# Kernel optimization log

Hardware: AMD Instinct MI355X
Metric: run time of the kernel (lower is better)

The kernel has to match this reference:

```python
import jax, jax.numpy as jnp
import numpy as np

N = 50000        # nodes
E = 800000       # edges (avg degree 16)
IN_DIM = 64
OUT_DIM = 64
SLOPE = 0.01     # torch F.leaky_relu default negative_slope


def setup_inputs() -> dict:
    key = jax.random.key(0)
    ks = jax.random.split(key, 11)
    v = jax.random.normal(ks[0], (N, IN_DIM), dtype=jnp.float32)
    pre_w = jax.random.uniform(ks[1], (E, 1), dtype=jnp.float32)
    src = jax.random.randint(ks[2], (E,), 0, N)
    dst = jax.random.randint(ks[3], (E,), 0, N)
    # learned params (Linear weights, stored [out_features, in_features] like torch)
    si = 1.0 / np.sqrt(IN_DIM)
    so = 1.0 / np.sqrt(OUT_DIM)
    Wa  = jax.random.normal(ks[4], (OUT_DIM, IN_DIM), dtype=jnp.float32) * si
    a_l = jax.random.normal(ks[5], (1, OUT_DIM), dtype=jnp.float32) * so
    a_r = jax.random.normal(ks[6], (1, OUT_DIM), dtype=jnp.float32) * so
    Wg  = jax.random.normal(ks[7], (OUT_DIM, IN_DIM), dtype=jnp.float32) * si
    gl  = jax.random.normal(ks[8], (1, IN_DIM), dtype=jnp.float32) * si
    gm  = jax.random.normal(ks[9], (1, OUT_DIM), dtype=jnp.float32) * so
    gr  = jax.random.normal(ks[10], (1, IN_DIM), dtype=jnp.float32) * si
    return {"v": v, "pre_w": pre_w, "src": src, "dst": dst,
            "Wa": Wa, "a_l": a_l, "a_r": a_r, "Wg": Wg,
            "gl": gl, "gm": gm, "gr": gr}


def reference(v, pre_w, src, dst, Wa, a_l, a_r, Wg, gl, gm, gr):
    # node projection: z = Wa(v)
    z = v @ Wa.T                                            # [N, OUT]
    # edge attention: e = leaky_relu(a_l(pre_w * z_src) + a_r(z_dst))
    s_r = z @ a_r.T                                         # [N, 1] (node-level right score)
    z_src = z[src]                                          # [E, OUT]
    e = jax.nn.leaky_relu(((pre_w * z_src) @ a_l.T + s_r[dst])[:, 0], SLOPE)  # [E]
    # segment softmax over in-edges of each dst node
    seg_max = jax.ops.segment_max(e, dst, num_segments=N)
    seg_max = jnp.where(jnp.isneginf(seg_max), 0.0, seg_max)
    ex = jnp.exp(e - seg_max[dst])                          # [E]
    denom = jax.ops.segment_sum(ex, dst, num_segments=N)    # [N]
    alpha = ex / jnp.maximum(denom[dst], 1e-16)             # [E]
    # attention-weighted aggregation of projected src features
    h = jax.ops.segment_sum(alpha[:, None] * z_src, dst, num_segments=N)  # [N, OUT]
    # gate path: pwFeat = pre_w * v_src, max over Wg(pwFeat), mean over pwFeat
    pwFeat = pre_w * v[src]                                 # [E, IN]
    gateProj = pwFeat @ Wg.T                                # [E, OUT]
    maxFeat = jax.ops.segment_max(gateProj, dst, num_segments=N)
    maxFeat = jnp.where(jnp.isneginf(maxFeat), 0.0, maxFeat)  # [N, OUT]
    cnt = jax.ops.segment_sum(jnp.ones((E,), jnp.float32), dst, num_segments=N)
    meanFeat = jax.ops.segment_sum(pwFeat, dst, num_segments=N) / jnp.maximum(cnt, 1.0)[:, None]
    gate = jax.nn.sigmoid(v @ gl.T + maxFeat @ gm.T + meanFeat @ gr.T)  # [N, 1]
    h = gate * h
    return h.reshape(1, N, OUT_DIM)  # batch_size = 1
```

## Files before the change

kernel.cpp:

```cpp
#include <hip/hip_runtime.h>
#include <hip/hip_fp16.h>

#define DIM 64
#define SLOPE 0.01f
#define P1_CHUNK 4096
#define CAP 8192
#define LDH 72

typedef _Float16 half8 __attribute__((ext_vector_type(8)));
typedef float float4v __attribute__((ext_vector_type(4)));

__global__ __launch_bounds__(256) void node_proj(
    const float* __restrict__ v, const float* __restrict__ Wa,
    const float* __restrict__ Wg, const float* __restrict__ a_l,
    const float* __restrict__ a_r, const float* __restrict__ gl,
    const float* __restrict__ gr,
    __half2* __restrict__ zu,
    float* __restrict__ s_l, float* __restrict__ s_r,
    float* __restrict__ t_gr, float* __restrict__ g0, int N)
{
    __shared__ _Float16 vt[64 * LDH];
    __shared__ _Float16 wah[64 * LDH];
    __shared__ _Float16 wgh[64 * LDH];
    __shared__ _Float16 bx[16 * LDH];
    int tid = threadIdx.x;
    int base = blockIdx.x * 64;

    {
        int r = tid >> 2, i0 = (tid & 3) * 16;
        int n = base + r;
        _Float16* dv = &vt[r * LDH + i0];
        if (n < N) {
            const float4* sv = (const float4*)(v + (size_t)n * DIM + i0);
#pragma unroll
            for (int c = 0; c < 4; c++) {
                float4 q = sv[c];
                dv[4*c+0] = (_Float16)q.x; dv[4*c+1] = (_Float16)q.y;
                dv[4*c+2] = (_Float16)q.z; dv[4*c+3] = (_Float16)q.w;
            }
        } else {
#pragma unroll
            for (int c = 0; c < 16; c++) dv[c] = (_Float16)0.f;
        }
        const float4* sa = (const float4*)(Wa + (size_t)r * DIM + i0);
        const float4* sg = (const float4*)(Wg + (size_t)r * DIM + i0);
        _Float16* da = &wah[r * LDH + i0];
        _Float16* dg = &wgh[r * LDH + i0];
#pragma unroll
        for (int c = 0; c < 4; c++) {
            float4 qa = sa[c], qg = sg[c];
            da[4*c+0] = (_Float16)qa.x; da[4*c+1] = (_Float16)qa.y;
            da[4*c+2] = (_Float16)qa.z; da[4*c+3] = (_Float16)qa.w;
            dg[4*c+0] = (_Float16)qg.x; dg[4*c+1] = (_Float16)qg.y;
            dg[4*c+2] = (_Float16)qg.z; dg[4*c+3] = (_Float16)qg.w;
        }
        if (tid < 64)       bx[0 * LDH + tid] = (_Float16)gl[tid];
        else if (tid < 128) bx[1 * LDH + (tid - 64)] = (_Float16)gr[tid - 64];
        for (int x = tid; x < 12 * 64; x += 256)
            bx[(4 + (x >> 6)) * LDH + (x & 63)] = (_Float16)0.f;
    }
    __syncthreads();
    if (tid < 64) {
        int i = tid;
        float acc = 0.f;
        for (int k = 0; k < 64; k++) acc = fmaf(a_l[k], (float)wah[k * LDH + i], acc);
        bx[2 * LDH + i] = (_Float16)acc;
    } else if (tid < 128) {
        int i = tid - 64;
        float acc = 0.f;
        for (int k = 0; k < 64; k++) acc = fmaf(a_r[k], (float)wah[k * LDH + i], acc);
        bx[3 * LDH + i] = (_Float16)acc;
    }
    __syncthreads();

    int lane = tid & 63;
    int m0 = (tid >> 6) * 16;
    int rb = lane & 15;
    int q  = lane >> 4;

    half8 a_lo = *(const half8*)&vt[(m0 + rb) * LDH + q * 8];
    half8 a_hi = *(const half8*)&vt[(m0 + rb) * LDH + 32 + q * 8];

    float4v zacc[4], uacc[4], sacc;
#pragma unroll
    for (int tc = 0; tc < 4; tc++) { zacc[tc] = (float4v)0.f; uacc[tc] = (float4v)0.f; }
    sacc = (float4v)0.f;

#pragma unroll
    for (int tc = 0; tc < 4; tc++) {
        int c0 = tc * 16;
        half8 blo = *(const half8*)&wah[(c0 + rb) * LDH + q * 8];
        half8 bhi = *(const half8*)&wah[(c0 + rb) * LDH + 32 + q * 8];
        zacc[tc] = __builtin_amdgcn_mfma_f32_16x16x32_f16(a_lo, blo, zacc[tc], 0, 0, 0);
        zacc[tc] = __builtin_amdgcn_mfma_f32_16x16x32_f16(a_hi, bhi, zacc[tc], 0, 0, 0);
        half8 glo = *(const half8*)&wgh[(c0 + rb) * LDH + q * 8];
        half8 ghi = *(const half8*)&wgh[(c0 + rb) * LDH + 32 + q * 8];
        uacc[tc] = __builtin_amdgcn_mfma_f32_16x16x32_f16(a_lo, glo, uacc[tc], 0, 0, 0);
        uacc[tc] = __builtin_amdgcn_mfma_f32_16x16x32_f16(a_hi, ghi, uacc[tc], 0, 0, 0);
    }
    {
        half8 blo = *(const half8*)&bx[rb * LDH + q * 8];
        half8 bhi = *(const half8*)&bx[rb * LDH + 32 + q * 8];
        sacc = __builtin_amdgcn_mfma_f32_16x16x32_f16(a_lo, blo, sacc, 0, 0, 0);
        sacc = __builtin_amdgcn_mfma_f32_16x16x32_f16(a_hi, bhi, sacc, 0, 0, 0);
    }

#pragma unroll
    for (int r = 0; r < 4; r++) {
        int n = base + m0 + q * 4 + r;
        if (n < N) {
#pragma unroll
            for (int tc = 0; tc < 4; tc++)
                zu[(size_t)n * DIM + tc * 16 + rb] = __floats2half2_rn(zacc[tc][r], uacc[tc][r]);
        }
    }
    if (rb < 4) {
        float* arr = (rb == 0) ? g0 : (rb == 1) ? t_gr : (rb == 2) ? s_l : s_r;
#pragma unroll
        for (int r = 0; r < 4; r++) {
            int n = base + m0 + q * 4 + r;
            if (n < N) arr[n] = sacc[r];
        }
    }
}

__global__ __launch_bounds__(256) void bucket_scatter(
    const int* __restrict__ src, const int* __restrict__ dst,
    const float* __restrict__ pre_w,
    int* __restrict__ bcur0, uint2* __restrict__ tmp, int E)
{
    __shared__ int h[256], lcur[256], wbase[256];
    int t = threadIdx.x;
    h[t] = 0; lcur[t] = 0;
    __syncthreads();
    int e0 = blockIdx.x * P1_CHUNK;
    int e1 = e0 + P1_CHUNK; if (e1 > E) e1 = E;
    for (int e = e0 + t; e < e1; e += 256)
        atomicAdd(&h[dst[e] >> 8], 1);
    __syncthreads();
    int hv = h[t];
    wbase[t] = hv ? atomicAdd(&bcur0[t], hv) : 0;
    __syncthreads();
    for (int e = e0 + t; e < e1; e += 256) {
        int d = dst[e];
        int b = d >> 8;
        int pos = wbase[b] + atomicAdd(&lcur[b], 1);
        if (pos < CAP) {
            unsigned lo = ((unsigned)src[e] << 16) |
                          __half_as_ushort(__float2half_rn(pre_w[e]));
            uint2 r; r.x = lo; r.y = (unsigned)d;
            tmp[(size_t)b * CAP + pos] = r;
        }
    }
}

__global__ __launch_bounds__(256) void bucket_to_csr(
    const uint2* __restrict__ tmp, const int* __restrict__ bcur0,
    int* __restrict__ offs, int* __restrict__ deg,
    unsigned int* __restrict__ sp_s, int N)
{
    __shared__ int h[256], excl[256], cur[256], sc[256];
    int b = blockIdx.x;
    int t = threadIdx.x;
    int c = bcur0[t]; if (c > CAP) c = CAP;
    sc[t] = c;
    __syncthreads();
    for (int off = 1; off < 256; off <<= 1) {
        int y = (t >= off) ? sc[t - off] : 0;
        __syncthreads();
        sc[t] += y;
        __syncthreads();
    }
    int start = (b == 0) ? 0 : sc[b - 1];
    int bcnt = sc[b] - start;
    const uint2* reg = tmp + (size_t)b * CAP;
    h[t] = 0; cur[t] = 0;
    __syncthreads();
    for (int i = t; i < bcnt; i += 256)
        atomicAdd(&h[reg[i].y & 255], 1);
    __syncthreads();
    int x = h[t];
    excl[t] = x;
    __syncthreads();
    for (int off = 1; off < 256; off <<= 1) {
        int y = (t >= off) ? excl[t - off] : 0;
        __syncthreads();
        excl[t] += y;
        __syncthreads();
    }
    int ex = excl[t] - x;
    int n = (b << 8) + t;
    if (n < N) { offs[n] = start + ex; deg[n] = x; }
    __syncthreads();
    excl[t] = ex;
    __syncthreads();
    for (int i = t; i < bcnt; i += 256) {
        uint2 r = reg[i];
        int d8 = r.y & 255;
        int pos = start + excl[d8] + atomicAdd(&cur[d8], 1);
        sp_s[pos] = r.x;
    }
}

__global__ __launch_bounds__(256) void aggregate(
    const int* __restrict__ offs, const int* __restrict__ deg_a,
    const unsigned int* __restrict__ sp_s,
    const __half2* __restrict__ zu,
    const float* __restrict__ s_l, const float* __restrict__ s_r,
    const float* __restrict__ t_gr, const float* __restrict__ g0,
    const float* __restrict__ gm,
    float* __restrict__ out, int N)
{
    int n = __builtin_amdgcn_readfirstlane((blockIdx.x * 256 + threadIdx.x) >> 6);
    int k = threadIdx.x & 63;
    if (n >= N) return;
    int deg = deg_a[n];
    size_t outIdx = (size_t)n * DIM + k;
    if (deg == 0) { out[outIdx] = 0.f; return; }
    int start = offs[n];
    float srn = s_r[n];

    float m = -INFINITY, denom = 0.f, hk = 0.f, mfk = -INFINITY, msum = 0.f;
    for (int c0 = 0; c0 < deg; c0 += 64) {
        int cn = deg - c0; if (cn > 64) cn = 64;
        unsigned rec = 0;
        float ea = -INFINITY;
        if (k < cn) {
            rec = sp_s[start + c0 + k];
            float pw = __half2float(__ushort_as_half((unsigned short)(rec & 0xffffu)));
            ea = fmaf(pw, s_l[rec >> 16], srn);
            ea = ea > 0.f ? ea : SLOPE * ea;
            msum = fmaf(pw, t_gr[rec >> 16], msum);
        }
        float mc = ea;
#pragma unroll
        for (int off = 32; off; off >>= 1) mc = fmaxf(mc, __shfl_xor(mc, off, 64));
        float mnew = fmaxf(m, mc);
        float scale = __expf(m - mnew);
        float w = __expf(ea - mnew);
        float sw = w;
#pragma unroll
        for (int off = 32; off; off >>= 1) sw += __shfl_xor(sw, off, 64);
        denom = denom * scale + sw;
        hk *= scale;
        m = mnew;
        int j = 0;
        for (; j + 8 <= cn; j += 8) {
            unsigned r8[8]; float w8[8]; __half2 q8[8];
#pragma unroll
            for (int i = 0; i < 8; i++) {
                r8[i] = __shfl(rec, j + i, 64);
                w8[i] = __shfl(w, j + i, 64);
            }
#pragma unroll
            for (int i = 0; i < 8; i++) q8[i] = zu[(size_t)(r8[i] >> 16) * DIM + k];
#pragma unroll
            for (int i = 0; i < 8; i++) {
                float2 f = __half22float2(q8[i]);
                float pwj = __half2float(__ushort_as_half((unsigned short)(r8[i] & 0xffffu)));
                hk = fmaf(w8[i], f.x, hk);
                mfk = fmaxf(mfk, pwj * f.y);
            }
        }
        for (; j < cn; j++) {
            unsigned rj = __shfl(rec, j, 64);
            float wj = __shfl(w, j, 64);
            __half2 q = zu[(size_t)(rj >> 16) * DIM + k];
            float2 f = __half22float2(q);
            float pwj = __half2float(__ushort_as_half((unsigned short)(rj & 0xffffu)));
            hk = fmaf(wj, f.x, hk);
            mfk = fmaxf(mfk, pwj * f.y);
        }
    }
#pragma unroll
    for (int off = 32; off; off >>= 1) msum += __shfl_xor(msum, off, 64);
    float r = gm[k] * mfk;
#pragma unroll
    for (int off = 32; off; off >>= 1) r += __shfl_down(r, off, 64);
    r = __shfl(r, 0, 64);
    float meanDot = msum / (float)deg;
    float xg = g0[n] + r + meanDot;
    float gate = 1.f / (1.f + __expf(-xg));
    out[outIdx] = gate * hk / fmaxf(denom, 1e-16f);
}

extern "C" void kernel_launch(void* const* d_in, const int* in_sizes, int n_in,
                              void* d_out, int out_size, void* d_ws, size_t ws_size,
                              hipStream_t stream)
{
    const float* v     = (const float*)d_in[0];
    const float* pre_w = (const float*)d_in[1];
    const int*   src   = (const int*)d_in[2];
    const int*   dst   = (const int*)d_in[3];
    const float* Wa    = (const float*)d_in[4];
    const float* a_l   = (const float*)d_in[5];
    const float* a_r   = (const float*)d_in[6];
    const float* Wg    = (const float*)d_in[7];
    const float* gl    = (const float*)d_in[8];
    const float* gm    = (const float*)d_in[9];
    const float* gr    = (const float*)d_in[10];
    int N = in_sizes[0] / DIM;
    int E = in_sizes[2];
    int nbuck = (N + 255) >> 8;

    char* ws    = (char*)d_ws;
    __half2* zu = (__half2*)ws;
    float* s_l  = (float*)(ws + (size_t)N * DIM * 4);
    float* s_r  = s_l + N;
    float* t_gr = s_r + N;
    float* g0   = t_gr + N;
    int* offs   = (int*)(g0 + N);
    int* deg    = offs + N;
    int* bcur0  = deg + N;
    uint2* tmp  = (uint2*)(bcur0 + 256);
    unsigned int* sp_s = (unsigned int*)(tmp + (size_t)nbuck * CAP);

    hipMemsetAsync(bcur0, 0, 256 * sizeof(int), stream);

    node_proj<<<(N + 63) / 64, 256, 0, stream>>>(
        v, Wa, Wg, a_l, a_r, gl, gr, zu, s_l, s_r, t_gr, g0, N);

    bucket_scatter<<<(E + P1_CHUNK - 1) / P1_CHUNK, 256, 0, stream>>>(
        src, dst, pre_w, bcur0, tmp, E);

    bucket_to_csr<<<nbuck, 256, 0, stream>>>(
        tmp, bcur0, offs, deg, sp_s, N);

    aggregate<<<(N + 3) / 4, 256, 0, stream>>>(
        offs, deg, sp_s, zu, s_l, s_r, t_gr, g0, gm, (float*)d_out, N);
}
```

Baseline: 168.1 us.

## Merge node projection and bucket scatter into one launch; interleave s_l and t_gr

```diff
diff --git a/kernel.cpp b/kernel.cpp
--- a/kernel.cpp
+++ b/kernel.cpp
@@ -10,21 +10,54 @@
 typedef _Float16 half8 __attribute__((ext_vector_type(8)));
 typedef float float4v __attribute__((ext_vector_type(4)));
 
-__global__ __launch_bounds__(256) void node_proj(
+__global__ __launch_bounds__(256) void proj_scatter(
     const float* __restrict__ v, const float* __restrict__ Wa,
     const float* __restrict__ Wg, const float* __restrict__ a_l,
     const float* __restrict__ a_r, const float* __restrict__ gl,
     const float* __restrict__ gr,
-    __half2* __restrict__ zu,
-    float* __restrict__ s_l, float* __restrict__ s_r,
-    float* __restrict__ t_gr, float* __restrict__ g0, int N)
+    __half2* __restrict__ zu, float2* __restrict__ st,
+    float* __restrict__ s_r, float* __restrict__ g0,
+    const int* __restrict__ src, const int* __restrict__ dst,
+    const float* __restrict__ pre_w,
+    int* __restrict__ bcur0, uint2* __restrict__ tmp,
+    int N, int E, int scBlocks)
 {
-    __shared__ _Float16 vt[64 * LDH];
-    __shared__ _Float16 wah[64 * LDH];
-    __shared__ _Float16 wgh[64 * LDH];
-    __shared__ _Float16 bx[16 * LDH];
+    __shared__ char smem[(64 * 3 + 16) * LDH * 2];
     int tid = threadIdx.x;
-    int base = blockIdx.x * 64;
+
+    if (blockIdx.x < scBlocks) {
+        int* h    = (int*)smem;
+        int* lcur = h + 256;
+        int* wbase = lcur + 256;
+        h[tid] = 0; lcur[tid] = 0;
+        __syncthreads();
+        int e0 = blockIdx.x * P1_CHUNK;
+        int e1 = e0 + P1_CHUNK; if (e1 > E) e1 = E;
+        for (int e = e0 + tid; e < e1; e += 256)
+            atomicAdd(&h[dst[e] >> 8], 1);
+        __syncthreads();
+        int hv = h[tid];
+        wbase[tid] = hv ? atomicAdd(&bcur0[tid], hv) : 0;
+        __syncthreads();
+        for (int e = e0 + tid; e < e1; e += 256) {
+            int d = dst[e];
+            int b = d >> 8;
+            int pos = wbase[b] + atomicAdd(&lcur[b], 1);
+            if (pos < CAP) {
+                unsigned lo = ((unsigned)src[e] << 16) |
+                              __half_as_ushort(__float2half_rn(pre_w[e]));
+                uint2 r; r.x = lo; r.y = (unsigned)d;
+                tmp[(size_t)b * CAP + pos] = r;
+            }
+        }
+        return;
+    }
+
+    _Float16* vt  = (_Float16*)smem;
+    _Float16* wah = vt + 64 * LDH;
+    _Float16* wgh = wah + 64 * LDH;
+    _Float16* bx  = wgh + 64 * LDH;
+    int base = (blockIdx.x - scBlocks) * 64;
 
     {
         int r = tid >> 2, i0 = (tid & 3) * 16;
@@ -115,41 +148,16 @@
         }
     }
     if (rb < 4) {
-        float* arr = (rb == 0) ? g0 : (rb == 1) ? t_gr : (rb == 2) ? s_l : s_r;
 #pragma unroll
         for (int r = 0; r < 4; r++) {
             int n = base + m0 + q * 4 + r;
-            if (n < N) arr[n] = sacc[r];
-        }
-    }
-}
-
-__global__ __launch_bounds__(256) void bucket_scatter(
-    const int* __restrict__ src, const int* __restrict__ dst,
-    const float* __restrict__ pre_w,
-    int* __restrict__ bcur0, uint2* __restrict__ tmp, int E)
-{
-    __shared__ int h[256], lcur[256], wbase[256];
-    int t = threadIdx.x;
-    h[t] = 0; lcur[t] = 0;
-    __syncthreads();
-    int e0 = blockIdx.x * P1_CHUNK;
-    int e1 = e0 + P1_CHUNK; if (e1 > E) e1 = E;
-    for (int e = e0 + t; e < e1; e += 256)
-        atomicAdd(&h[dst[e] >> 8], 1);
-    __syncthreads();
-    int hv = h[t];
-    wbase[t] = hv ? atomicAdd(&bcur0[t], hv) : 0;
-    __syncthreads();
-    for (int e = e0 + t; e < e1; e += 256) {
-        int d = dst[e];
-        int b = d >> 8;
-        int pos = wbase[b] + atomicAdd(&lcur[b], 1);
-        if (pos < CAP) {
-            unsigned lo = ((unsigned)src[e] << 16) |
-                          __half_as_ushort(__float2half_rn(pre_w[e]));
-            uint2 r; r.x = lo; r.y = (unsigned)d;
-            tmp[(size_t)b * CAP + pos] = r;
+            if (n < N) {
+                float val = sacc[r];
+                if (rb == 0) g0[n] = val;
+                else if (rb == 1) st[n].y = val;
+                else if (rb == 2) st[n].x = val;
+                else s_r[n] = val;
+            }
         }
     }
 }
@@ -206,9 +214,8 @@
     const int* __restrict__ offs, const int* __restrict__ deg_a,
     const unsigned int* __restrict__ sp_s,
     const __half2* __restrict__ zu,
-    const float* __restrict__ s_l, const float* __restrict__ s_r,
-    const float* __restrict__ t_gr, const float* __restrict__ g0,
-    const float* __restrict__ gm,
+    const float2* __restrict__ st, const float* __restrict__ s_r,
+    const float* __restrict__ g0, const float* __restrict__ gm,
     float* __restrict__ out, int N)
 {
     int n = __builtin_amdgcn_readfirstlane((blockIdx.x * 256 + threadIdx.x) >> 6);
@@ -227,10 +234,11 @@
         float ea = -INFINITY;
         if (k < cn) {
             rec = sp_s[start + c0 + k];
+            float2 stv = st[rec >> 16];
             float pw = __half2float(__ushort_as_half((unsigned short)(rec & 0xffffu)));
-            ea = fmaf(pw, s_l[rec >> 16], srn);
+            ea = fmaf(pw, stv.x, srn);
             ea = ea > 0.f ? ea : SLOPE * ea;
-            msum = fmaf(pw, t_gr[rec >> 16], msum);
+            msum = fmaf(pw, stv.y, msum);
         }
         float mc = ea;
 #pragma unroll
@@ -302,13 +310,14 @@
     int N = in_sizes[0] / DIM;
     int E = in_sizes[2];
     int nbuck = (N + 255) >> 8;
+    int scBlocks = (E + P1_CHUNK - 1) / P1_CHUNK;
+    int npBlocks = (N + 63) / 64;
 
     char* ws    = (char*)d_ws;
     __half2* zu = (__half2*)ws;
-    float* s_l  = (float*)(ws + (size_t)N * DIM * 4);
-    float* s_r  = s_l + N;
-    float* t_gr = s_r + N;
-    float* g0   = t_gr + N;
+    float2* st  = (float2*)(ws + (size_t)N * DIM * 4);
+    float* s_r  = (float*)(st + N);
+    float* g0   = s_r + N;
     int* offs   = (int*)(g0 + N);
     int* deg    = offs + N;
     int* bcur0  = deg + N;
@@ -317,15 +326,13 @@
 
     hipMemsetAsync(bcur0, 0, 256 * sizeof(int), stream);
 
-    node_proj<<<(N + 63) / 64, 256, 0, stream>>>(
-        v, Wa, Wg, a_l, a_r, gl, gr, zu, s_l, s_r, t_gr, g0, N);
-
-    bucket_scatter<<<(E + P1_CHUNK - 1) / P1_CHUNK, 256, 0, stream>>>(
-        src, dst, pre_w, bcur0, tmp, E);
+    proj_scatter<<<scBlocks + npBlocks, 256, 0, stream>>>(
+        v, Wa, Wg, a_l, a_r, gl, gr, zu, st, s_r, g0,
+        src, dst, pre_w, bcur0, tmp, N, E, scBlocks);
 
     bucket_to_csr<<<nbuck, 256, 0, stream>>>(
         tmp, bcur0, offs, deg, sp_s, N);
 
     aggregate<<<(N + 3) / 4, 256, 0, stream>>>(
-        offs, deg, sp_s, zu, s_l, s_r, t_gr, g0, gm, (float*)d_out, N);
+        offs, deg, sp_s, zu, st, s_r, g0, gm, (float*)d_out, N);
 }
```

New measurement: 158.1 us, median of 2. 1.06x faster.
